# Kernel tuning notes

Measured on AMD Instinct MI355X. Metric: run time of the kernel, lower is better.

Reference implementation:

```python
import jax, jax.numpy as jnp
import numpy as np

E, H, I, K, T = 8, 1024, 2816, 2, 2048


def setup_inputs() -> dict:
    key = jax.random.key(0)
    k1, k2, k3, k4, k5, k6 = jax.random.split(key, 6)
    hidden_states = jax.random.normal(k1, (T, H), dtype=jnp.float32)
    top_k_indices = jax.random.randint(k2, (T, K), 0, E, dtype=jnp.int32)
    raw = jax.random.uniform(k3, (T, K), dtype=jnp.float32) + 0.1
    top_k_values = raw / jnp.sum(raw, axis=-1, keepdims=True)  # router softmax-like weights
    scale = 1.0 / np.sqrt(H)
    w_gate = jax.random.normal(k4, (E, H, I), dtype=jnp.float32) * scale
    w_up = jax.random.normal(k5, (E, H, I), dtype=jnp.float32) * scale
    w_down = jax.random.normal(k6, (E, I, H), dtype=jnp.float32) * (1.0 / np.sqrt(I))
    return {
        "hidden_states": hidden_states,
        "top_k_indices": top_k_indices,
        "top_k_values": top_k_values,
        "w_gate": w_gate,
        "w_up": w_up,
        "w_down": w_down,
    }


def reference(hidden_states, top_k_indices, top_k_values, w_gate, w_up, w_down):
    # Each expert: SwiGLU FFN  down( silu(x @ gate) * (x @ up) )
    # Run every expert on every token (dense reference for grouped-GEMM dispatch),
    # then combine with the per-token top-k routing weights.
    def expert(wg, wu, wd):
        g = jnp.matmul(hidden_states, wg)          # [T, I]
        u = jnp.matmul(hidden_states, wu)          # [T, I]
        return jnp.matmul(jax.nn.silu(g) * u, wd)  # [T, H]

    y = jax.vmap(expert)(w_gate, w_up, w_down)     # [E, T, H]

    t = hidden_states.shape[0]
    # comb[t, e] = sum over k of top_k_values[t, k] where top_k_indices[t, k] == e
    comb = jnp.zeros((t, w_gate.shape[0]), dtype=hidden_states.dtype)
    comb = comb.at[jnp.arange(t)[:, None], top_k_indices].add(top_k_values)
    out = jnp.einsum('te,eth->th', comb, y)        # weighted combine -> [T, H]
    return out
```

## Files before the change

kernel.cpp:

```cpp
#include <hip/hip_runtime.h>
#include <stdint.h>

#define T_TOK 2048
#define KTOP  2
#define NEXP  8
#define HDIM  1024
#define IDIM  2816

#define NPAIR 4096

#define BM        128
#define MAX_TILES 40
#define NPP       (NPAIR + BM)
#define BN2       128
#define BK2       32
#define BN3       128
#define BK3       64
#define NYH       11
#define GUBH      (MAX_TILES * NYH)
#define CVT       5632

#define R1BM   256
#define R1T    24
#define R1NPP  (NPAIR + R1BM)
#define R1BN2  128
#define R1BK2  32
#define R1BKp2 40
#define R1BN3  64
#define R1BK3  64
#define R1BKp3 72

typedef __attribute__((ext_vector_type(8))) short short8;
typedef __attribute__((ext_vector_type(4))) float floatx4;

__device__ __forceinline__ unsigned short f2bf(float f) {
  unsigned int u = __float_as_uint(f);
  u += 0x7fffu + ((u >> 16) & 1u);
  return (unsigned short)(u >> 16);
}

__device__ __forceinline__ unsigned int pkbf(float a, float b) {
  unsigned int r;
  asm volatile("v_cvt_pk_bf16_f32 %0, %1, %2" : "=v"(r) : "v"(a), "v"(b));
  return r;
}

__device__ __forceinline__ void glds16(const unsigned short* g, unsigned short* l) {
  __builtin_amdgcn_global_load_lds(
      (const __attribute__((address_space(1))) unsigned int*)g,
      (__attribute__((address_space(3))) unsigned int*)l, 16, 0, 0);
}

__device__ __forceinline__ int xcd_tile(int bx0) {
  return (bx0 & 7) * (MAX_TILES / 8) + (bx0 >> 3);
}

__global__ void setup_kernel(const int* __restrict__ idx,
                             const float* __restrict__ vals,
                             int* __restrict__ hdr,
                             int* __restrict__ stok,
                             float* __restrict__ sw, int bm) {
  __shared__ int cnt[NEXP];
  __shared__ int off[NEXP];
  int tid = threadIdx.x;
  if (tid < NEXP) cnt[tid] = 0;
  __syncthreads();
  for (int p = tid; p < NPAIR; p += blockDim.x) atomicAdd(&cnt[idx[p]], 1);
  __syncthreads();
  if (tid == 0) {
    int s = 0, nt = 0;
    for (int e = 0; e < NEXP; ++e) {
      off[e] = s;
      int n = cnt[e];
      for (int t0 = 0; t0 < n; t0 += bm) {
        hdr[nt] = e;
        hdr[64 + nt] = s + t0;
        hdr[128 + nt] = s + n;
        nt++;
      }
      s += n;
    }
    for (; nt < 64; ++nt) hdr[nt] = -1;
  }
  __syncthreads();
  for (int p = tid; p < NPAIR; p += blockDim.x) {
    int e = idx[p];
    int pos = atomicAdd(&off[e], 1);
    stok[pos] = p / KTOP;
    sw[pos] = vals[p];
  }
}

__global__ void gather_kernel(const float* __restrict__ hidden,
                              const int* __restrict__ stok,
                              unsigned short* __restrict__ Xs) {
  int p = blockIdx.x;
  int t = stok[p];
  const float4* src = reinterpret_cast<const float4*>(hidden + (size_t)t * HDIM);
  float4 v = src[threadIdx.x];
  uint2 q;
  q.x = pkbf(v.x, v.y);
  q.y = pkbf(v.z, v.w);
  *reinterpret_cast<uint2*>(Xs + (size_t)p * HDIM + threadIdx.x * 4) = q;
}

__global__ __launch_bounds__(256) void convert_kernel(
    const float* __restrict__ wg, const float* __restrict__ wu,
    const float* __restrict__ wd, unsigned short* __restrict__ wgT,
    unsigned short* __restrict__ wuT, unsigned short* __restrict__ wdT,
    int zoff, int ioff, int intx) {
  __shared__ float ls[64][65];
  int z = blockIdx.z + zoff;
  int e = blockIdx.y;
  int M = (z == 2) ? IDIM : HDIM;
  int N = (z == 2) ? HDIM : IDIM;
  const float* src = (z == 0 ? wg : z == 1 ? wu : wd) + (size_t)e * M * N;
  unsigned short* dst = (z == 0 ? wgT : z == 1 ? wuT : wdT) + (size_t)e * M * N;
  int n0 = ((blockIdx.x % intx) + ioff) << 6;
  int m0 = (blockIdx.x / intx) << 6;
  int t = threadIdx.x;
  int rr = t >> 4, cc = (t & 15) * 4;
#pragma unroll
  for (int i = 0; i < 4; ++i) {
    int r = rr + i * 16;
    float4 v = *reinterpret_cast<const float4*>(src + (size_t)(m0 + r) * N + n0 + cc);
    ls[r][cc] = v.x; ls[r][cc + 1] = v.y; ls[r][cc + 2] = v.z; ls[r][cc + 3] = v.w;
  }
  __syncthreads();
  int mc = (t & 7) * 8, nn = t >> 3;
#pragma unroll
  for (int i = 0; i < 2; ++i) {
    int n = nn + i * 32;
    uint4 q;
    q.x = pkbf(ls[mc][n],     ls[mc + 1][n]);
    q.y = pkbf(ls[mc + 2][n], ls[mc + 3][n]);
    q.z = pkbf(ls[mc + 4][n], ls[mc + 5][n]);
    q.w = pkbf(ls[mc + 6][n], ls[mc + 7][n]);
    *reinterpret_cast<uint4*>(dst + (size_t)(n0 + n) * M + m0 + mc) = q;
  }
}

__global__ __launch_bounds__(256, 2) void gateup_kernel(
    const unsigned short* __restrict__ Xs, const unsigned short* __restrict__ wgT,
    const unsigned short* __restrict__ wuT, const int* __restrict__ hdr,
    const float* __restrict__ sw_g, unsigned short* __restrict__ Act,
    const float* __restrict__ wg, const float* __restrict__ wu,
    const float* __restrict__ wd, unsigned short* __restrict__ wgTw,
    unsigned short* __restrict__ wuTw, unsigned short* __restrict__ wdTw,
    int mode) {
  __shared__ __align__(16) char smem[25088];

  if (blockIdx.x >= GUBH) {
    int cb = blockIdx.x - GUBH;
    const float* src;
    unsigned short* dst;
    int n0, m0, rdN, wrM;
    if (mode == 0) {
      int z = cb / 2816;
      int rem = cb - z * 2816;
      int e = rem / 352;
      int bq = rem % 352;
      n0 = ((bq % 22) + 22) << 6;
      m0 = (bq / 22) << 6;
      rdN = IDIM; wrM = HDIM;
      src = (z ? wu : wg) + (size_t)e * HDIM * IDIM;
      dst = (z ? wuTw : wgTw) + (size_t)e * IDIM * HDIM;
    } else {
      int e = cb / 704;
      int bq = cb % 704;
      n0 = (bq % 16) << 6;
      m0 = (bq / 16) << 6;
      rdN = HDIM; wrM = IDIM;
      src = wd + (size_t)e * IDIM * HDIM;
      dst = wdTw + (size_t)e * IDIM * HDIM;
    }
    float (*ls)[65] = reinterpret_cast<float(*)[65]>(smem);
    int t = threadIdx.x;
    int rr = t >> 4, cc = (t & 15) * 4;
#pragma unroll
    for (int i = 0; i < 4; ++i) {
      int r = rr + i * 16;
      float4 v = *reinterpret_cast<const float4*>(src + (size_t)(m0 + r) * rdN + n0 + cc);
      ls[r][cc] = v.x; ls[r][cc + 1] = v.y; ls[r][cc + 2] = v.z; ls[r][cc + 3] = v.w;
    }
    __syncthreads();
    int mc = (t & 7) * 8, nn = t >> 3;
#pragma unroll
    for (int i = 0; i < 2; ++i) {
      int n = nn + i * 32;
      uint4 q;
      q.x = pkbf(ls[mc][n],     ls[mc + 1][n]);
      q.y = pkbf(ls[mc + 2][n], ls[mc + 3][n]);
      q.z = pkbf(ls[mc + 4][n], ls[mc + 5][n]);
      q.w = pkbf(ls[mc + 6][n], ls[mc + 7][n]);
      *reinterpret_cast<uint4*>(dst + (size_t)(n0 + n) * wrM + m0 + mc) = q;
    }
    return;
  }

  int mx = blockIdx.x % MAX_TILES;
  int ny = blockIdx.x / MAX_TILES + mode * NYH;
  int bx = xcd_tile(mx);
  int e = hdr[bx];
  if (e < 0) return;
  int row0 = hdr[64 + bx];
  int rowlim = hdr[128 + bx] - row0;
  int n0 = ny * BN2;

  unsigned short* As = reinterpret_cast<unsigned short*>(smem);
  unsigned short* Bg = reinterpret_cast<unsigned short*>(smem + 8192);
  unsigned short* Bu = reinterpret_cast<unsigned short*>(smem + 16384);
  float* sw = reinterpret_cast<float*>(smem + 24576);

  int tid = threadIdx.x, lane = tid & 63, wave = tid >> 6;
  if (tid < BM) sw[tid] = sw_g[row0 + tid];

  const unsigned short* wgb = wgT + (size_t)e * IDIM * HDIM;
  const unsigned short* wub = wuT + (size_t)e * IDIM * HDIM;

  floatx4 accg[4][4], accu[4][4];
  floatx4 zz = {0.f, 0.f, 0.f, 0.f};
#pragma unroll
  for (int a = 0; a < 4; ++a)
#pragma unroll
    for (int b = 0; b < 4; ++b) { accg[a][b] = zz; accu[a][b] = zz; }

  int wm = (wave >> 1) * 64, wn = (wave & 1) * 64;
  int lr = lane >> 2;
  int lk = (((lane & 3) ^ ((lr >> 1) & 3)) * 8);
  int fr = lane & 15;
  int fq = (((lane >> 4) ^ ((fr >> 1) & 3)) * 8);

  for (int kb = 0; kb < HDIM; kb += BK2) {
#pragma unroll
    for (int it = 0; it < 2; ++it) {
      int c = wave * 2 + it;
      glds16(Xs  + (size_t)(row0 + c * 16 + lr) * HDIM + kb + lk, &As[c * 512]);
      glds16(wgb + (size_t)(n0  + c * 16 + lr) * HDIM + kb + lk, &Bg[c * 512]);
      glds16(wub + (size_t)(n0  + c * 16 + lr) * HDIM + kb + lk, &Bu[c * 512]);
    }
    __syncthreads();

    short8 af[4], bg8[4], bu8[4];
#pragma unroll
    for (int x = 0; x < 4; ++x) {
      af[x]  = *reinterpret_cast<const short8*>(&As[(wm + x * 16 + fr) * BK2 + fq]);
      bg8[x] = *reinterpret_cast<const short8*>(&Bg[(wn + x * 16 + fr) * BK2 + fq]);
      bu8[x] = *reinterpret_cast<const short8*>(&Bu[(wn + x * 16 + fr) * BK2 + fq]);
    }
#pragma unroll
    for (int tm = 0; tm < 4; ++tm)
#pragma unroll
      for (int tn = 0; tn < 4; ++tn) {
        accg[tm][tn] = __builtin_amdgcn_mfma_f32_16x16x32_bf16(af[tm], bg8[tn], accg[tm][tn], 0, 0, 0);
        accu[tm][tn] = __builtin_amdgcn_mfma_f32_16x16x32_bf16(af[tm], bu8[tn], accu[tm][tn], 0, 0, 0);
      }
    __syncthreads();
  }

#pragma unroll
  for (int tm = 0; tm < 4; ++tm)
#pragma unroll
    for (int tn = 0; tn < 4; ++tn)
#pragma unroll
      for (int r = 0; r < 4; ++r) {
        int rl = wm + tm * 16 + (lane >> 4) * 4 + r;
        if (rl < rowlim) {
          int col = n0 + wn + tn * 16 + fr;
          float g = accg[tm][tn][r];
          float u = accu[tm][tn][r];
          float s = g / (1.f + __expf(-g));
          Act[(size_t)(row0 + rl) * IDIM + col] = f2bf(s * u * sw[rl]);
        }
      }
}

__global__ __launch_bounds__(256, 4) void down_kernel(
    const unsigned short* __restrict__ Act, const unsigned short* __restrict__ wdT,
    const int* __restrict__ hdr, const int* __restrict__ stok,
    float* __restrict__ out) {
  int bx = xcd_tile(blockIdx.x);
  int e = hdr[bx];
  if (e < 0) return;
  int row0 = hdr[64 + bx];
  int rowlim = hdr[128 + bx] - row0;
  int n0 = blockIdx.y * BN3;
  int kb0 = blockIdx.z * (IDIM / 2);
  int kend = kb0 + (IDIM / 2);

  __shared__ __align__(16) unsigned short As[BM * BK3];
  __shared__ __align__(16) unsigned short Bd[BN3 * BK3];
  __shared__ int stk[BM];

  int tid = threadIdx.x, lane = tid & 63, wave = tid >> 6;
  if (tid < BM) stk[tid] = stok[row0 + tid];

  const unsigned short* wdb = wdT + (size_t)e * HDIM * IDIM;

  floatx4 acc[4][4];
  floatx4 zz = {0.f, 0.f, 0.f, 0.f};
#pragma unroll
  for (int a = 0; a < 4; ++a)
#pragma unroll
    for (int b = 0; b < 4; ++b) acc[a][b] = zz;

  int wm = (wave >> 1) * 64, wn = (wave & 1) * 64;
  int lr8 = lane >> 3;
  int lk8 = (((lane & 7) ^ lr8) * 8);
  int fr = lane & 15;
  int fk = fr & 7;

  for (int kb = kb0; kb < kend; kb += BK3) {
#pragma unroll
    for (int it = 0; it < 4; ++it) {
      int c = wave * 4 + it;
      glds16(Act + (size_t)(row0 + c * 8 + lr8) * IDIM + kb + lk8, &As[c * 512]);
      glds16(wdb + (size_t)(n0  + c * 8 + lr8) * IDIM + kb + lk8, &Bd[c * 512]);
    }
    __syncthreads();

#pragma unroll
    for (int ks = 0; ks < BK3; ks += 32) {
      int q8 = (ks >> 3) + (lane >> 4);
      int fo = ((q8 ^ fk) * 8);
      short8 af[4], bd8[4];
#pragma unroll
      for (int x = 0; x < 4; ++x) {
        af[x]  = *reinterpret_cast<const short8*>(&As[(wm + x * 16 + fr) * BK3 + fo]);
        bd8[x] = *reinterpret_cast<const short8*>(&Bd[(wn + x * 16 + fr) * BK3 + fo]);
      }
#pragma unroll
      for (int tm = 0; tm < 4; ++tm)
#pragma unroll
        for (int tn = 0; tn < 4; ++tn)
          acc[tm][tn] = __builtin_amdgcn_mfma_f32_16x16x32_bf16(af[tm], bd8[tn], acc[tm][tn], 0, 0, 0);
    }
    __syncthreads();
  }

#pragma unroll
  for (int tm = 0; tm < 4; ++tm)
#pragma unroll
    for (int tn = 0; tn < 4; ++tn)
#pragma unroll
      for (int r = 0; r < 4; ++r) {
        int rl = wm + tm * 16 + (lane >> 4) * 4 + r;
        if (rl < rowlim) {
          int col = n0 + wn + tn * 16 + fr;
          unsafeAtomicAdd(&out[(size_t)stk[rl] * HDIM + col], acc[tm][tn][r]);
        }
      }
}

__global__ __launch_bounds__(512, 2) void gateup_fb(
    const unsigned short* __restrict__ Xs, const float* __restrict__ wg,
    const float* __restrict__ wu, const int* __restrict__ hdr,
    const float* __restrict__ sw_g, unsigned short* __restrict__ Act) {
  int by = blockIdx.y;
  int e = hdr[by];
  if (e < 0) return;
  int row0 = hdr[64 + by];
  int row_end = hdr[128 + by];
  int n0 = blockIdx.x * R1BN2;

  __shared__ __align__(16) unsigned short As[R1BM * R1BKp2];
  __shared__ __align__(16) unsigned short Bg[R1BN2 * R1BKp2];
  __shared__ __align__(16) unsigned short Bu[R1BN2 * R1BKp2];
  __shared__ float sw[R1BM];

  int tid = threadIdx.x, lane = tid & 63, wave = tid >> 6;
  if (tid < R1BM) sw[tid] = sw_g[row0 + tid];

  const float* wgb = wg + (size_t)e * HDIM * IDIM;
  const float* wub = wu + (size_t)e * HDIM * IDIM;

  floatx4 accg[4][4], accu[4][4];
  floatx4 zz = {0.f, 0.f, 0.f, 0.f};
#pragma unroll
  for (int a = 0; a < 4; ++a)
#pragma unroll
    for (int b = 0; b < 4; ++b) { accg[a][b] = zz; accu[a][b] = zz; }

  int wm = (wave >> 1) * 64, wn = (wave & 1) * 64;

  for (int kb = 0; kb < HDIM; kb += R1BK2) {
    __syncthreads();
#pragma unroll
    for (int it = 0; it < 2; ++it) {
      int cc = wave * 2 + it;
      int m = cc * 16 + (lane >> 2);
      int k = (lane & 3) * 8;
      uint4 v = *reinterpret_cast<const uint4*>(Xs + (size_t)(row0 + m) * HDIM + kb + k);
      *reinterpret_cast<uint4*>(&As[m * R1BKp2 + k]) = v;
    }
#pragma unroll
    for (int it = 0; it < 2; ++it) {
      int cc = wave * 2 + it;
      const float* wb = (cc & 8) ? wub : wgb;
      unsigned short* Bs = (cc & 8) ? Bu : Bg;
      int r = cc & 7;
      int kblk = r >> 1, nh = r & 1;
      int n = nh * 64 + lane;
      int k = kblk * 8;
      const float* src = wb + (size_t)(kb + k) * IDIM + n0 + n;
      uint4 q;
      q.x = f2bf(src[0])                | ((unsigned)f2bf(src[(size_t)IDIM])     << 16);
      q.y = f2bf(src[2 * (size_t)IDIM]) | ((unsigned)f2bf(src[3 * (size_t)IDIM]) << 16);
      q.z = f2bf(src[4 * (size_t)IDIM]) | ((unsigned)f2bf(src[5 * (size_t)IDIM]) << 16);
      q.w = f2bf(src[6 * (size_t)IDIM]) | ((unsigned)f2bf(src[7 * (size_t)IDIM]) << 16);
      *reinterpret_cast<uint4*>(&Bs[n * R1BKp2 + k]) = q;
    }
    __syncthreads();

    int krd = (lane >> 4) * 8;
    short8 af[4], bgf[4], buf_[4];
#pragma unroll
    for (int tm = 0; tm < 4; ++tm)
      af[tm] = *reinterpret_cast<const short8*>(&As[(wm + tm * 16 + (lane & 15)) * R1BKp2 + krd]);
#pragma unroll
    for (int tn = 0; tn < 4; ++tn) {
      bgf[tn]  = *reinterpret_cast<const short8*>(&Bg[(wn + tn * 16 + (lane & 15)) * R1BKp2 + krd]);
      buf_[tn] = *reinterpret_cast<const short8*>(&Bu[(wn + tn * 16 + (lane & 15)) * R1BKp2 + krd]);
    }
#pragma unroll
    for (int tm = 0; tm < 4; ++tm)
#pragma unroll
      for (int tn = 0; tn < 4; ++tn) {
        accg[tm][tn] = __builtin_amdgcn_mfma_f32_16x16x32_bf16(af[tm], bgf[tn], accg[tm][tn], 0, 0, 0);
        accu[tm][tn] = __builtin_amdgcn_mfma_f32_16x16x32_bf16(af[tm], buf_[tn], accu[tm][tn], 0, 0, 0);
      }
  }

  int rowlim = row_end - row0;
#pragma unroll
  for (int tm = 0; tm < 4; ++tm)
#pragma unroll
    for (int tn = 0; tn < 4; ++tn)
#pragma unroll
      for (int r = 0; r < 4; ++r) {
        int rl = wm + tm * 16 + (lane >> 4) * 4 + r;
        if (rl < rowlim) {
          int col = n0 + wn + tn * 16 + (lane & 15);
          float g = accg[tm][tn][r];
          float u = accu[tm][tn][r];
          float s = g / (1.f + __expf(-g));
          Act[(size_t)(row0 + rl) * IDIM + col] = f2bf(s * u * sw[rl]);
        }
      }
}

__global__ __launch_bounds__(512, 2) void down_fb(
    const unsigned short* __restrict__ Act, const float* __restrict__ wd,
    const int* __restrict__ hdr, const int* __restrict__ stok,
    float* __restrict__ out) {
  int by = blockIdx.y;
  int e = hdr[by];
  if (e < 0) return;
  int row0 = hdr[64 + by];
  int row_end = hdr[128 + by];
  int n0 = blockIdx.x * R1BN3;

  __shared__ __align__(16) unsigned short As[R1BM * R1BKp3];
  __shared__ __align__(16) unsigned short Bd[R1BN3 * R1BKp3];
  __shared__ int stk[R1BM];

  int tid = threadIdx.x, lane = tid & 63, wave = tid >> 6;
  if (tid < R1BM) stk[tid] = stok[row0 + tid];

  const float* wdb = wd + (size_t)e * IDIM * HDIM;

  floatx4 acc[4][2];
  floatx4 zz = {0.f, 0.f, 0.f, 0.f};
#pragma unroll
  for (int a = 0; a < 4; ++a) { acc[a][0] = zz; acc[a][1] = zz; }

  int wm = (wave >> 1) * 64, wn = (wave & 1) * 32;

  for (int kb = 0; kb < IDIM; kb += R1BK3) {
    __syncthreads();
#pragma unroll
    for (int it = 0; it < 4; ++it) {
      int cc = wave * 4 + it;
      int m = cc * 8 + (lane >> 3);
      int k = (lane & 7) * 8;
      uint4 v = *reinterpret_cast<const uint4*>(Act + (size_t)(row0 + m) * IDIM + kb + k);
      *reinterpret_cast<uint4*>(&As[m * R1BKp3 + k]) = v;
    }
    {
      int n = lane;
      int k = wave * 8;
      const float* src = wdb + (size_t)(kb + k) * HDIM + n0 + n;
      uint4 q;
      q.x = f2bf(src[0])        | ((unsigned)f2bf(src[HDIM])     << 16);
      q.y = f2bf(src[2 * HDIM]) | ((unsigned)f2bf(src[3 * HDIM]) << 16);
      q.z = f2bf(src[4 * HDIM]) | ((unsigned)f2bf(src[5 * HDIM]) << 16);
      q.w = f2bf(src[6 * HDIM]) | ((unsigned)f2bf(src[7 * HDIM]) << 16);
      *reinterpret_cast<uint4*>(&Bd[n * R1BKp3 + k]) = q;
    }
    __syncthreads();

#pragma unroll
    for (int ks = 0; ks < R1BK3; ks += 32) {
      int krd = ks + (lane >> 4) * 8;
      short8 af[4], bdf[2];
#pragma unroll
      for (int tm = 0; tm < 4; ++tm)
        af[tm] = *reinterpret_cast<const short8*>(&As[(wm + tm * 16 + (lane & 15)) * R1BKp3 + krd]);
#pragma unroll
      for (int tn = 0; tn < 2; ++tn)
        bdf[tn] = *reinterpret_cast<const short8*>(&Bd[(wn + tn * 16 + (lane & 15)) * R1BKp3 + krd]);
#pragma unroll
      for (int tm = 0; tm < 4; ++tm)
#pragma unroll
        for (int tn = 0; tn < 2; ++tn)
          acc[tm][tn] = __builtin_amdgcn_mfma_f32_16x16x32_bf16(af[tm], bdf[tn], acc[tm][tn], 0, 0, 0);
    }
  }

  int rowlim = row_end - row0;
#pragma unroll
  for (int tm = 0; tm < 4; ++tm)
#pragma unroll
    for (int tn = 0; tn < 2; ++tn)
#pragma unroll
      for (int r = 0; r < 4; ++r) {
        int rl = wm + tm * 16 + (lane >> 4) * 4 + r;
        if (rl < rowlim) {
          int col = n0 + wn + tn * 16 + (lane & 15);
          unsafeAtomicAdd(&out[(size_t)stk[rl] * HDIM + col], acc[tm][tn][r]);
        }
      }
}

extern "C" void kernel_launch(void* const* d_in, const int* in_sizes, int n_in,
                              void* d_out, int out_size, void* d_ws, size_t ws_size,
                              hipStream_t stream) {
  const float* hidden = (const float*)d_in[0];
  const int* idx = (const int*)d_in[1];
  const float* vals = (const float*)d_in[2];
  const float* wg = (const float*)d_in[3];
  const float* wu = (const float*)d_in[4];
  const float* wd = (const float*)d_in[5];
  float* out = (float*)d_out;
  char* ws = (char*)d_ws;

  hipMemsetAsync(d_out, 0, (size_t)out_size * sizeof(float), stream);

  const size_t OFF_STOK = 4096;
  const size_t OFF_SW   = OFF_STOK + (size_t)NPP * 4;
  const size_t OFF_XS   = 65536;
  const size_t OFF_ACT  = OFF_XS + (size_t)NPP * HDIM * 2;
  const size_t OFF_WG   = OFF_ACT + (size_t)NPP * IDIM * 2;
  const size_t WSZ      = (size_t)NEXP * HDIM * IDIM * 2;
  const size_t OFF_WU   = OFF_WG + WSZ;
  const size_t OFF_WD   = OFF_WU + WSZ;
  const size_t NEED     = OFF_WD;
  const size_t NEED2    = OFF_WD + WSZ;

  if (ws_size >= NEED) {
    int* hdr = (int*)ws;
    int* stok = (int*)(ws + OFF_STOK);
    float* sw = (float*)(ws + OFF_SW);
    unsigned short* Xs  = (unsigned short*)(ws + OFF_XS);
    unsigned short* Act = (unsigned short*)(ws + OFF_ACT);
    unsigned short* wgT = (unsigned short*)(ws + OFF_WG);
    unsigned short* wuT = (unsigned short*)(ws + OFF_WU);
    bool sep = (ws_size >= NEED2);
    unsigned short* wdT = sep ? (unsigned short*)(ws + OFF_WD) : wgT;

    setup_kernel<<<1, 1024, 0, stream>>>(idx, vals, hdr, stok, sw, BM);
    convert_kernel<<<dim3(352, NEXP, 2), 256, 0, stream>>>(
        wg, wu, wd, wgT, wuT, wdT, 0, 0, 22);
    gather_kernel<<<NPAIR, 256, 0, stream>>>(hidden, stok, Xs);
    gateup_kernel<<<GUBH + CVT, 256, 0, stream>>>(
        Xs, wgT, wuT, hdr, sw, Act, wg, wu, wd, wgT, wuT, wdT, 0);
    if (sep) {
      gateup_kernel<<<GUBH + CVT, 256, 0, stream>>>(
          Xs, wgT, wuT, hdr, sw, Act, wg, wu, wd, wgT, wuT, wdT, 1);
    } else {
      gateup_kernel<<<GUBH, 256, 0, stream>>>(
          Xs, wgT, wuT, hdr, sw, Act, wg, wu, wd, wgT, wuT, wdT, 1);
      convert_kernel<<<dim3(704, NEXP, 1), 256, 0, stream>>>(
          wg, wu, wd, wgT, wuT, wdT, 2, 0, 16);
    }
    down_kernel<<<dim3(MAX_TILES, HDIM / BN3, 2), 256, 0, stream>>>(
        Act, wdT, hdr, stok, out);
  } else {
    int* hdr = (int*)ws;
    int* stok = (int*)(ws + 4096);
    float* sw = (float*)(ws + 4096 + (size_t)R1NPP * 4);
    unsigned short* Xs  = (unsigned short*)(ws + 65536);
    unsigned short* Act = (unsigned short*)(ws + 65536 + (size_t)R1NPP * HDIM * 2);

    setup_kernel<<<1, 1024, 0, stream>>>(idx, vals, hdr, stok, sw, R1BM);
    gather_kernel<<<NPAIR, 256, 0, stream>>>(hidden, stok, Xs);
    gateup_fb<<<dim3(IDIM / R1BN2, R1T), 512, 0, stream>>>(Xs, wg, wu, hdr, sw, Act);
    down_fb<<<dim3(HDIM / R1BN3, R1T), 512, 0, stream>>>(Act, wd, hdr, stok, out);
  }
}
```

Measured before the change: 420.2 us.

## Coarsen weight-convert blocks with prefetch and fuse first convert with gather

Weight transpose/convert work is restructured so each block converts a stack of eight or eleven 64x64 tiles, with the next tile's loads issued before the current tile's writes. This cuts the number of convert blocks and overlaps global reads with shared-memory transposes. The first half gate/up conversion and the token gather are fused into one prep kernel, which removes one launch. Fewer, heavier blocks can leave tail imbalance and reduce overlap with the co-scheduled GEMM blocks.

```diff
diff --git a/kernel.cpp b/kernel.cpp
--- a/kernel.cpp
+++ b/kernel.cpp
@@ -18,7 +18,8 @@
 #define BK3       64
 #define NYH       11
 #define GUBH      (MAX_TILES * NYH)
-#define CVT       5632
+#define CVH       704
+#define CVZ2      512
 
 #define R1BM   256
 #define R1T    24
@@ -53,6 +54,60 @@
 
 __device__ __forceinline__ int xcd_tile(int bx0) {
   return (bx0 & 7) * (MAX_TILES / 8) + (bx0 >> 3);
+}
+
+__device__ __forceinline__ void conv_fat(
+    const float* __restrict__ src, unsigned short* __restrict__ dst,
+    int rdN, int wrM, int m0, int n0, int nt, float (*ls)[65]) {
+  int t = threadIdx.x;
+  int rr = t >> 4, cc = (t & 15) * 4;
+  int mc = (t & 7) * 8, nn = t >> 3;
+  float4 v[4], w[4];
+#pragma unroll
+  for (int i = 0; i < 4; ++i)
+    v[i] = *reinterpret_cast<const float4*>(src + (size_t)(m0 + rr + i * 16) * rdN + n0 + cc);
+  for (int tt = 0; tt < nt; ++tt) {
+    int m0t = m0 + tt * 64;
+    __syncthreads();
+#pragma unroll
+    for (int i = 0; i < 4; ++i) {
+      int r = rr + i * 16;
+      ls[r][cc] = v[i].x; ls[r][cc + 1] = v[i].y;
+      ls[r][cc + 2] = v[i].z; ls[r][cc + 3] = v[i].w;
+    }
+    if (tt + 1 < nt) {
+#pragma unroll
+      for (int i = 0; i < 4; ++i)
+        w[i] = *reinterpret_cast<const float4*>(src + (size_t)(m0t + 64 + rr + i * 16) * rdN + n0 + cc);
+    }
+    __syncthreads();
+#pragma unroll
+    for (int i = 0; i < 2; ++i) {
+      int n = nn + i * 32;
+      uint4 q;
+      q.x = pkbf(ls[mc][n],     ls[mc + 1][n]);
+      q.y = pkbf(ls[mc + 2][n], ls[mc + 3][n]);
+      q.z = pkbf(ls[mc + 4][n], ls[mc + 5][n]);
+      q.w = pkbf(ls[mc + 6][n], ls[mc + 7][n]);
+      *reinterpret_cast<uint4*>(dst + (size_t)(n0 + n) * wrM + m0t + mc) = q;
+    }
+#pragma unroll
+    for (int i = 0; i < 4; ++i) v[i] = w[i];
+  }
+}
+
+__device__ __forceinline__ void conv_z01_half(
+    int cb, int ioff, const float* wg, const float* wu,
+    unsigned short* wgT, unsigned short* wuT, float (*ls)[65]) {
+  int z = cb / 352;
+  int rem = cb - z * 352;
+  int e = rem / 44;
+  int r2 = rem % 44;
+  int mg = r2 / 22;
+  int it = r2 % 22;
+  const float* src = (z ? wu : wg) + (size_t)e * HDIM * IDIM;
+  unsigned short* dst = (z ? wuT : wgT) + (size_t)e * IDIM * HDIM;
+  conv_fat(src, dst, IDIM, HDIM, mg * 512, (it + ioff) * 64, 8, ls);
 }
 
 __global__ void setup_kernel(const int* __restrict__ idx,
@@ -104,6 +159,27 @@
   *reinterpret_cast<uint2*>(Xs + (size_t)p * HDIM + threadIdx.x * 4) = q;
 }
 
+__global__ __launch_bounds__(256) void prep_kernel(
+    const float* __restrict__ hidden, const int* __restrict__ stok,
+    unsigned short* __restrict__ Xs, const float* __restrict__ wg,
+    const float* __restrict__ wu, unsigned short* __restrict__ wgT,
+    unsigned short* __restrict__ wuT) {
+  __shared__ float ls[64][65];
+  int bx = blockIdx.x;
+  if (bx < CVH) {
+    conv_z01_half(bx, 0, wg, wu, wgT, wuT, ls);
+    return;
+  }
+  int p = bx - CVH;
+  int t = stok[p];
+  const float4* src = reinterpret_cast<const float4*>(hidden + (size_t)t * HDIM);
+  float4 v = src[threadIdx.x];
+  uint2 q;
+  q.x = pkbf(v.x, v.y);
+  q.y = pkbf(v.z, v.w);
+  *reinterpret_cast<uint2*>(Xs + (size_t)p * HDIM + threadIdx.x * 4) = q;
+}
+
 __global__ __launch_bounds__(256) void convert_kernel(
     const float* __restrict__ wg, const float* __restrict__ wu,
     const float* __restrict__ wd, unsigned short* __restrict__ wgT,
@@ -118,26 +194,7 @@
   unsigned short* dst = (z == 0 ? wgT : z == 1 ? wuT : wdT) + (size_t)e * M * N;
   int n0 = ((blockIdx.x % intx) + ioff) << 6;
   int m0 = (blockIdx.x / intx) << 6;
-  int t = threadIdx.x;
-  int rr = t >> 4, cc = (t & 15) * 4;
-#pragma unroll
-  for (int i = 0; i < 4; ++i) {
-    int r = rr + i * 16;
-    float4 v = *reinterpret_cast<const float4*>(src + (size_t)(m0 + r) * N + n0 + cc);
-    ls[r][cc] = v.x; ls[r][cc + 1] = v.y; ls[r][cc + 2] = v.z; ls[r][cc + 3] = v.w;
-  }
-  __syncthreads();
-  int mc = (t & 7) * 8, nn = t >> 3;
-#pragma unroll
-  for (int i = 0; i < 2; ++i) {
-    int n = nn + i * 32;
-    uint4 q;
-    q.x = pkbf(ls[mc][n],     ls[mc + 1][n]);
-    q.y = pkbf(ls[mc + 2][n], ls[mc + 3][n]);
-    q.z = pkbf(ls[mc + 4][n], ls[mc + 5][n]);
-    q.w = pkbf(ls[mc + 6][n], ls[mc + 7][n]);
-    *reinterpret_cast<uint4*>(dst + (size_t)(n0 + n) * M + m0 + mc) = q;
-  }
+  conv_fat(src, dst, N, M, m0, n0, 1, ls);
 }
 
 __global__ __launch_bounds__(256, 2) void gateup_kernel(
@@ -152,48 +209,16 @@
 
   if (blockIdx.x >= GUBH) {
     int cb = blockIdx.x - GUBH;
-    const float* src;
-    unsigned short* dst;
-    int n0, m0, rdN, wrM;
+    float (*ls)[65] = reinterpret_cast<float(*)[65]>(smem);
     if (mode == 0) {
-      int z = cb / 2816;
-      int rem = cb - z * 2816;
-      int e = rem / 352;
-      int bq = rem % 352;
-      n0 = ((bq % 22) + 22) << 6;
-      m0 = (bq / 22) << 6;
-      rdN = IDIM; wrM = HDIM;
-      src = (z ? wu : wg) + (size_t)e * HDIM * IDIM;
-      dst = (z ? wuTw : wgTw) + (size_t)e * IDIM * HDIM;
+      conv_z01_half(cb, 22, wg, wu, wgTw, wuTw, ls);
     } else {
-      int e = cb / 704;
-      int bq = cb % 704;
-      n0 = (bq % 16) << 6;
-      m0 = (bq / 16) << 6;
-      rdN = HDIM; wrM = IDIM;
-      src = wd + (size_t)e * IDIM * HDIM;
-      dst = wdTw + (size_t)e * IDIM * HDIM;
-    }
-    float (*ls)[65] = reinterpret_cast<float(*)[65]>(smem);
-    int t = threadIdx.x;
-    int rr = t >> 4, cc = (t & 15) * 4;
-#pragma unroll
-    for (int i = 0; i < 4; ++i) {
-      int r = rr + i * 16;
-      float4 v = *reinterpret_cast<const float4*>(src + (size_t)(m0 + r) * rdN + n0 + cc);
-      ls[r][cc] = v.x; ls[r][cc + 1] = v.y; ls[r][cc + 2] = v.z; ls[r][cc + 3] = v.w;
-    }
-    __syncthreads();
-    int mc = (t & 7) * 8, nn = t >> 3;
-#pragma unroll
-    for (int i = 0; i < 2; ++i) {
-      int n = nn + i * 32;
-      uint4 q;
-      q.x = pkbf(ls[mc][n],     ls[mc + 1][n]);
-      q.y = pkbf(ls[mc + 2][n], ls[mc + 3][n]);
-      q.z = pkbf(ls[mc + 4][n], ls[mc + 5][n]);
-      q.w = pkbf(ls[mc + 6][n], ls[mc + 7][n]);
-      *reinterpret_cast<uint4*>(dst + (size_t)(n0 + n) * wrM + m0 + mc) = q;
+      int e = cb / 64;
+      int rem = cb % 64;
+      int mg = rem / 16;
+      int it = rem % 16;
+      conv_fat(wd + (size_t)e * IDIM * HDIM, wdTw + (size_t)e * IDIM * HDIM,
+               HDIM, IDIM, mg * 704, it * 64, 11, ls);
     }
     return;
   }
@@ -569,13 +594,12 @@
     unsigned short* wdT = sep ? (unsigned short*)(ws + OFF_WD) : wgT;
 
     setup_kernel<<<1, 1024, 0, stream>>>(idx, vals, hdr, stok, sw, BM);
-    convert_kernel<<<dim3(352, NEXP, 2), 256, 0, stream>>>(
-        wg, wu, wd, wgT, wuT, wdT, 0, 0, 22);
-    gather_kernel<<<NPAIR, 256, 0, stream>>>(hidden, stok, Xs);
-    gateup_kernel<<<GUBH + CVT, 256, 0, stream>>>(
+    prep_kernel<<<CVH + NPAIR, 256, 0, stream>>>(
+        hidden, stok, Xs, wg, wu, wgT, wuT);
+    gateup_kernel<<<GUBH + CVH, 256, 0, stream>>>(
         Xs, wgT, wuT, hdr, sw, Act, wg, wu, wd, wgT, wuT, wdT, 0);
     if (sep) {
-      gateup_kernel<<<GUBH + CVT, 256, 0, stream>>>(
+      gateup_kernel<<<GUBH + CVZ2, 256, 0, stream>>>(
           Xs, wgT, wuT, hdr, sw, Act, wg, wu, wd, wgT, wuT, wdT, 1);
     } else {
       gateup_kernel<<<GUBH, 256, 0, stream>>>(
```

Measured after the change: 423.1 us. Within noise of the previous version (+0.7%).
